# Performance work log

Hardware: AMD Instinct MI355X
Metric: run time of the kernel (lower is better)

## Reference

```python
import jax, jax.numpy as jnp
import numpy as np

D = 1024   # n_embd
H = 16     # n_head
NL = 6     # n_layer
B = 16
L = 64
T = 3 * L  # interleaved (rtg, state, action) tokens
NB = 100   # rtg bucket number
DF = 4 * D


def _ln(x, g, b, eps=1e-5):
    mu = jnp.mean(x, -1, keepdims=True)
    var = jnp.mean((x - mu) ** 2, -1, keepdims=True)
    return (x - mu) * jax.lax.rsqrt(var + eps) * g + b


def _gelu(x):
    return jax.nn.gelu(x, approximate=False)  # matches torch F.gelu (erf)


def setup_inputs() -> dict:
    key = jax.random.key(0)
    ks = iter(jax.random.split(key, 64))
    def rn(shape, s=0.02):
        return jax.random.normal(next(ks), shape, jnp.float32) * s
    inp = dict(
        states=jax.random.normal(next(ks), (B, L, 91), jnp.float32),
        actions=jax.random.normal(next(ks), (B, L, 1, 27), jnp.float32),
        rtgs=jax.random.uniform(next(ks), (B, L), jnp.float32) * 100.0,
        attention_mask=jnp.ones((B, L), bool),
        y_len=L,
        # state encoder: Linear(91,D) GELU Linear(D,D) GELU
        se_w1=rn((91, D)), se_b1=jnp.zeros(D), se_w2=rn((D, D)), se_b2=jnp.zeros(D),
        # action encoder: Linear(27,D) GELU Linear(D,D)
        ae_w1=rn((27, D)), ae_b1=jnp.zeros(D), ae_w2=rn((D, D)), ae_b2=jnp.zeros(D),
        # Autodis
        ad_bucket_w=rn((1, D)), ad_bucket_b=jnp.zeros(D), ad_ret_w=rn((1, NB)), ad_res_w=rn((NB, NB)),
        pos_emb=rn((1, T, D)),
        # transformer blocks (stacked over layers)
        ln1_g=jnp.ones((NL, D)), ln1_b=jnp.zeros((NL, D)),
        Wq=rn((NL, D, D)), bq=jnp.zeros((NL, D)),
        Wk=rn((NL, D, D)), bk=jnp.zeros((NL, D)),
        Wv=rn((NL, D, D)), bv=jnp.zeros((NL, D)),
        Wp=rn((NL, D, D)), bp=jnp.zeros((NL, D)),
        ln2_g=jnp.ones((NL, D)), ln2_b=jnp.zeros((NL, D)),
        Wm1=rn((NL, D, DF)), bm1=jnp.zeros((NL, DF)),
        Wm2=rn((NL, DF, D)), bm2=jnp.zeros((NL, D)),
        lin_w=rn((D, 27)), lin_b=jnp.zeros(27),
    )
    return inp


def _forward(attention_mask, states, actions, rtgs, se_w1, se_b1, se_w2, se_b2,
             ae_w1, ae_b1, ae_w2, ae_b2, ad_bucket_w, ad_bucket_b, ad_ret_w, ad_res_w,
             pos_emb, ln1_g, ln1_b, Wq, bq, Wk, bk, Wv, bv, Wp, bp,
             ln2_g, ln2_b, Wm1, bm1, Wm2, bm2, lin_w, lin_b):
    Bsz, Ls = states.shape[0], states.shape[1]
    Ts = 3 * Ls
    hd = D // H
    # encoders
    state_emb = _gelu(_gelu(states @ se_w1 + se_b1) @ se_w2 + se_b2)          # [B,L,D]
    act = actions[:, :, 0, :]                                                  # squeeze(2) -> [B,L,27]
    action_emb = _gelu(act @ ae_w1 + ae_b1) @ ae_w2 + ae_b2                    # [B,L,D]
    # Autodis rtg embedding
    bucket_value = jnp.linspace(0.0, 100.0, NB).reshape(NB, 1)
    meta = bucket_value @ ad_bucket_w + ad_bucket_b                            # [NB,D]
    s = jax.nn.leaky_relu(rtgs[..., None] @ ad_ret_w)                          # [B,L,NB]
    s = s + s @ ad_res_w
    e = jnp.exp(s - jnp.max(s, -1, keepdims=True))
    p = e / (1e-8 + jnp.sum(e, -1, keepdims=True))
    rtg_emb = p @ meta                                                         # [B,L,D]
    # interleave rtg/state/action tokens -> [B,3L,D]
    tok = jnp.stack([rtg_emb, state_emb, action_emb], axis=2).reshape(Bsz, Ts, D)
    x = tok + pos_emb[:, :Ts]
    # combined padding + causal mask
    m = jnp.repeat(attention_mask, 3, axis=1)                                  # [B,3L]
    causal = jnp.tril(jnp.ones((Ts, Ts), bool))
    fmask = m[:, None, :, None] & m[:, None, None, :] & causal[None, None]     # [B,1,T,T]
    scale = 1.0 / np.sqrt(hd)
    for i in range(NL):
        h = _ln(x, ln1_g[i], ln1_b[i])
        q = (h @ Wq[i] + bq[i]).reshape(Bsz, Ts, H, hd).transpose(0, 2, 1, 3)
        k = (h @ Wk[i] + bk[i]).reshape(Bsz, Ts, H, hd).transpose(0, 2, 1, 3)
        v = (h @ Wv[i] + bv[i]).reshape(Bsz, Ts, H, hd).transpose(0, 2, 1, 3)
        att = jnp.einsum('bhid,bhjd->bhij', q, k) * scale
        att = jnp.where(fmask, att, -1e9)
        att = jax.nn.softmax(att, axis=-1)
        y = jnp.einsum('bhij,bhjd->bhid', att, v).transpose(0, 2, 1, 3).reshape(Bsz, Ts, D)
        x = x + (y @ Wp[i] + bp[i])
        h2 = _ln(x, ln2_g[i], ln2_b[i])
        x = x + _gelu(h2 @ Wm1[i] + bm1[i]) @ Wm2[i] + bm2[i]
    return x @ lin_w + lin_b                                                   # [B,3L,27]


def reference(states, actions, rtgs, attention_mask, y_len, se_w1, se_b1, se_w2, se_b2,
              ae_w1, ae_b1, ae_w2, ae_b2, ad_bucket_w, ad_bucket_b, ad_ret_w, ad_res_w,
              pos_emb, ln1_g, ln1_b, Wq, bq, Wk, bk, Wv, bv, Wp, bp,
              ln2_g, ln2_b, Wm1, bm1, Wm2, bm2, lin_w, lin_b):
    return _forward(attention_mask, states, actions, rtgs, se_w1, se_b1, se_w2, se_b2,
                    ae_w1, ae_b1, ae_w2, ae_b2, ad_bucket_w, ad_bucket_b, ad_ret_w, ad_res_w,
                    pos_emb, ln1_g, ln1_b, Wq, bq, Wk, bk, Wv, bv, Wp, bp,
                    ln2_g, ln2_b, Wm1, bm1, Wm2, bm2, lin_w, lin_b)
```

## Files before the change

kernel.cpp:

```cpp
#include <hip/hip_runtime.h>
#include <cmath>

typedef unsigned short u16;
typedef unsigned int   u32;
typedef short s16x8 __attribute__((ext_vector_type(8)));
typedef float f32x4 __attribute__((ext_vector_type(4)));

#define D_  1024
#define H_  16
#define NL_ 6
#define B_  16
#define L_  64
#define T_  192
#define NB_ 100
#define DF_ 4096
#define BT_ (B_*T_)
#define BL_ (B_*L_)

__device__ __forceinline__ float b2f(u16 u){ u32 x = ((u32)u)<<16; return __uint_as_float(x); }
__device__ __forceinline__ u16 f2b(float f){ u32 x = __float_as_uint(f); x += 0x7fffu + ((x>>16)&1u); return (u16)(x>>16); }
__device__ __forceinline__ float gelu_f(float v){ return 0.5f*v*(1.0f+erff(v*0.70710678118f)); }

typedef const unsigned int __attribute__((address_space(1)))* as1_u32p;
typedef unsigned int __attribute__((address_space(3)))* as3_u32p;
__device__ __forceinline__ void gload16(const void* g, void* l)
{
    __builtin_amdgcn_global_load_lds((as1_u32p)g, (as3_u32p)l, 16, 0, 0);
}

__global__ __launch_bounds__(256) void tconv_kernel(const float* __restrict__ W,
                                                    u16* __restrict__ Wt,
                                                    int K, int N,
                                                    size_t inLS, size_t outLS)
{
    __shared__ float tile[64][65];
    int tid = threadIdx.x;
    int nb = blockIdx.x * 64, kb = blockIdx.y * 64;
    const float* Wz = W + blockIdx.z * inLS;
    u16* Wtz = Wt + blockIdx.z * outLS;
    int tr = tid >> 4, tc = tid & 15;
#pragma unroll
    for (int rr = 0; rr < 4; ++rr) {
        int k = tr + rr*16;
        float4 v = *(const float4*)(Wz + (size_t)(kb + k)*N + nb + tc*4);
        tile[k][tc*4+0] = v.x; tile[k][tc*4+1] = v.y;
        tile[k][tc*4+2] = v.z; tile[k][tc*4+3] = v.w;
    }
    __syncthreads();
#pragma unroll
    for (int rr = 0; rr < 4; ++rr) {
        int n = tr + rr*16;
        ushort4 o;
        o.x = f2b(tile[tc*4+0][n]);
        o.y = f2b(tile[tc*4+1][n]);
        o.z = f2b(tile[tc*4+2][n]);
        o.w = f2b(tile[tc*4+3][n]);
        *(ushort4*)(Wtz + (size_t)(nb + n)*K + kb + tc*4) = o;
    }
}

__global__ __launch_bounds__(256) void tconv4_kernel(const float* __restrict__ Wq,
                                                     const float* __restrict__ Wk,
                                                     const float* __restrict__ Wv,
                                                     const float* __restrict__ Wp,
                                                     u16* __restrict__ Wqkvt,
                                                     u16* __restrict__ Wpt)
{
    __shared__ float tile[64][65];
    int tid = threadIdx.x;
    int z = blockIdx.z;
    int sel = z / NL_, layer = z - sel*NL_;
    size_t DD = (size_t)D_*D_;
    const float* Wz = ((sel == 0) ? Wq : (sel == 1) ? Wk : (sel == 2) ? Wv : Wp) + layer*DD;
    u16* Wtz = (sel == 3) ? (Wpt + layer*DD) : (Wqkvt + layer*3*DD + sel*DD);
    int nb = blockIdx.x * 64, kb = blockIdx.y * 64;
    int tr = tid >> 4, tc = tid & 15;
#pragma unroll
    for (int rr = 0; rr < 4; ++rr) {
        int k = tr + rr*16;
        float4 v = *(const float4*)(Wz + (size_t)(kb + k)*D_ + nb + tc*4);
        tile[k][tc*4+0] = v.x; tile[k][tc*4+1] = v.y;
        tile[k][tc*4+2] = v.z; tile[k][tc*4+3] = v.w;
    }
    __syncthreads();
#pragma unroll
    for (int rr = 0; rr < 4; ++rr) {
        int n = tr + rr*16;
        ushort4 o;
        o.x = f2b(tile[tc*4+0][n]);
        o.y = f2b(tile[tc*4+1][n]);
        o.z = f2b(tile[tc*4+2][n]);
        o.w = f2b(tile[tc*4+3][n]);
        *(ushort4*)(Wtz + (size_t)(nb + n)*D_ + kb + tc*4) = o;
    }
}

__global__ __launch_bounds__(256) void pack_qkv_bias_kernel(const float* __restrict__ bq,
                                                            const float* __restrict__ bk,
                                                            const float* __restrict__ bv,
                                                            float* __restrict__ out)
{
    int i = blockIdx.x*256 + threadIdx.x;
    int layer = i / 3072;
    int r = i - layer*3072;
    int c = r >> 10, d = r & 1023;
    const float* src = (c == 0) ? bq : (c == 1) ? bk : bv;
    out[i] = src[layer*1024 + d];
}

__global__ __launch_bounds__(256) void tlin_kernel(const float* __restrict__ w,
                                                   float* __restrict__ wt)
{
    int k = blockIdx.x*256 + threadIdx.x;
#pragma unroll 1
    for (int c = 0; c < 27; ++c)
        wt[c*1024 + k] = w[k*27 + c];
}

__global__ __launch_bounds__(256) void embed1_kernel(const float* __restrict__ A,
                                                     const float* __restrict__ W,
                                                     const float* __restrict__ bias,
                                                     u16* __restrict__ out, int K)
{
    int idx = blockIdx.x*256 + threadIdx.x;
    int m = idx >> 10, n = idx & 1023;
    float acc = bias[n];
    for (int k = 0; k < K; ++k)
        acc += A[m*K + k] * W[k*1024 + n];
    out[idx] = f2b(gelu_f(acc));
}

__global__ __launch_bounds__(128) void rtg_kernel(const float* __restrict__ rtgs,
                                                  const float* __restrict__ ret_w,
                                                  const float* __restrict__ res_w,
                                                  const float* __restrict__ bucket_w,
                                                  const float* __restrict__ bucket_b,
                                                  float* __restrict__ eR)
{
    int r = blockIdx.x, tid = threadIdx.x;
    __shared__ float sarr[NB_];
    __shared__ float red[128];
    float rtg = rtgs[r];
    float s = 0.f;
    if (tid < NB_) {
        float v = rtg * ret_w[tid];
        s = (v > 0.f) ? v : 0.01f*v;
        sarr[tid] = s;
    }
    __syncthreads();
    float s2 = -1e30f;
    if (tid < NB_) {
        float acc = s;
        for (int m = 0; m < NB_; ++m) acc += sarr[m] * res_w[m*NB_ + tid];
        s2 = acc;
    }
    red[tid] = s2; __syncthreads();
    for (int off = 64; off > 0; off >>= 1) { if (tid < off) red[tid] = fmaxf(red[tid], red[tid+off]); __syncthreads(); }
    float mx = red[0]; __syncthreads();
    float e = (tid < NB_) ? expf(s2 - mx) : 0.f;
    red[tid] = e; __syncthreads();
    for (int off = 64; off > 0; off >>= 1) { if (tid < off) red[tid] += red[tid+off]; __syncthreads(); }
    float S = red[0]; __syncthreads();
    float bv = (100.f/99.f) * (float)tid;
    red[tid] = e * bv; __syncthreads();
    for (int off = 64; off > 0; off >>= 1) { if (tid < off) red[tid] += red[tid+off]; __syncthreads(); }
    float EB = red[0];
    float inv = 1.f/(1e-8f + S);
    float c = EB * inv, sg = S * inv;
    for (int d = tid; d < D_; d += 128)
        eR[(size_t)r*D_ + d] = c*bucket_w[d] + sg*bucket_b[d];
}

__global__ __launch_bounds__(256) void assemble_kernel(const float* __restrict__ eR,
                                                       const float* __restrict__ eS,
                                                       const float* __restrict__ eA,
                                                       const float* __restrict__ pos,
                                                       float* __restrict__ xf)
{
    int idx = blockIdx.x*256 + threadIdx.x;
    int row = idx >> 10, d = idx & 1023;
    int b = row / T_, t = row % T_;
    int l = t / 3, c = t % 3;
    const float* src = (c == 0) ? eR : (c == 1) ? eS : eA;
    xf[idx] = src[(size_t)(b*L_ + l)*D_ + d] + pos[(size_t)t*D_ + d];
}

template<int NP>
__global__ __launch_bounds__(256) void ln_kernel(const float* __restrict__ x,
                                                 const float* __restrict__ p0,
                                                 const float* __restrict__ p1,
                                                 const float* __restrict__ g,
                                                 const float* __restrict__ bb,
                                                 float* __restrict__ xout,
                                                 u16* __restrict__ out)
{
    int row = blockIdx.x, tid = threadIdx.x;
    int lane = tid & 63, wv = tid >> 6;
    __shared__ float ps[8];
    float4 v = ((const float4*)(x + (size_t)row*D_))[tid];
    if (NP == 2) {
        float4 a = ((const float4*)(p0 + (size_t)row*D_))[tid];
        float4 b = ((const float4*)(p1 + (size_t)row*D_))[tid];
        v.x += a.x + b.x; v.y += a.y + b.y; v.z += a.z + b.z; v.w += a.w + b.w;
        ((float4*)(xout + (size_t)row*D_))[tid] = v;
    }
    float s = v.x+v.y+v.z+v.w;
    float q = v.x*v.x+v.y*v.y+v.z*v.z+v.w*v.w;
#pragma unroll
    for (int off = 1; off < 64; off <<= 1) {
        s += __shfl_xor(s, off, 64);
        q += __shfl_xor(q, off, 64);
    }
    if (lane == 0) { ps[wv] = s; ps[4+wv] = q; }
    __syncthreads();
    s = ps[0]+ps[1]+ps[2]+ps[3];
    q = ps[4]+ps[5]+ps[6]+ps[7];
    float mean = s*(1.f/(float)D_);
    float var  = q*(1.f/(float)D_) - mean*mean;
    float rstd = rsqrtf(var + 1e-5f);
    int d0 = tid*4;
    ushort4 ov;
    ov.x = f2b((v.x-mean)*rstd*g[d0+0] + bb[d0+0]);
    ov.y = f2b((v.y-mean)*rstd*g[d0+1] + bb[d0+1]);
    ov.z = f2b((v.z-mean)*rstd*g[d0+2] + bb[d0+2]);
    ov.w = f2b((v.w-mean)*rstd*g[d0+3] + bb[d0+3]);
    ((ushort4*)(out + (size_t)row*D_))[tid] = ov;
}

template<int GELU_ACT, int SPLITK, int ATOMIC>
__global__ __launch_bounds__(256) void gemm_bt(const u16* __restrict__ A,
                                               const u16* __restrict__ Bt,
                                               const float* __restrict__ bias,
                                               float* __restrict__ outF,
                                               u16* __restrict__ outB,
                                               int M, int N, int K, int kc,
                                               size_t partStride)
{
    __shared__ __align__(16) u16 As[3*128*32];
    __shared__ __align__(16) u16 Bs[3*128*32];
    int tid = threadIdx.x;

    int gx = gridDim.x;
    int nwg = gx * gridDim.y;
    int id = blockIdx.y * gx + blockIdx.x;
    int q8 = nwg >> 3;
    int nid = (id & 7) * q8 + (id >> 3);
    int n0 = (nid % gx) * 128;
    int m0 = (nid / gx) * 128;

    int wave = tid >> 6, lane = tid & 63;
    int wm = (wave >> 1) * 64, wn = (wave & 1) * 64;
    int lr = lane & 15, lq = lane >> 4;
    int slotRd = (lq ^ ((lr >> 1) & 3)) * 8;

    int srow = tid >> 2;
    int sslot = (tid & 3) ^ ((srow >> 1) & 3);

    int k0 = (SPLITK > 1) ? blockIdx.z * kc : 0;
    int nIt = ((SPLITK > 1) ? kc : K) >> 5;

    const u16* ap0 = A  + (size_t)(m0 + srow) * K + k0 + sslot * 8;
    const u16* ap1 = ap0 + (size_t)64 * K;
    const u16* bp0 = Bt + (size_t)(n0 + srow) * K + k0 + sslot * 8;
    const u16* bp1 = bp0 + (size_t)64 * K;

    u16 *sA0 = As, *sA1 = As + 4096, *sA2 = As + 8192;
    u16 *sB0 = Bs, *sB1 = Bs + 4096, *sB2 = Bs + 8192;
    int woff = wave * 512;

    f32x4 acc[4][4];
#pragma unroll
    for (int i = 0; i < 4; ++i)
#pragma unroll
        for (int j = 0; j < 4; ++j) acc[i][j] = (f32x4){0.f,0.f,0.f,0.f};

    gload16(ap0, sA0 + woff); gload16(ap1, sA0 + 2048 + woff);
    gload16(bp0, sB0 + woff); gload16(bp1, sB0 + 2048 + woff);
    ap0 += 32; ap1 += 32; bp0 += 32; bp1 += 32;
    gload16(ap0, sA1 + woff); gload16(ap1, sA1 + 2048 + woff);
    gload16(bp0, sB1 + woff); gload16(bp1, sB1 + 2048 + woff);
    ap0 += 32; ap1 += 32; bp0 += 32; bp1 += 32;

    for (int it = 0; it < nIt; ++it) {
        if (it + 1 < nIt) asm volatile("s_waitcnt vmcnt(4)" ::: "memory");
        else              asm volatile("s_waitcnt vmcnt(0)" ::: "memory");
        asm volatile("s_barrier" ::: "memory");
        if (it + 2 < nIt) {
            gload16(ap0, sA2 + woff); gload16(ap1, sA2 + 2048 + woff);
            gload16(bp0, sB2 + woff); gload16(bp1, sB2 + 2048 + woff);
            ap0 += 32; ap1 += 32; bp0 += 32; bp1 += 32;
        }
        s16x8 af[4], bf[4];
#pragma unroll
        for (int i = 0; i < 4; ++i)
            af[i] = *(const s16x8*)(sA0 + (wm + i*16 + lr)*32 + slotRd);
#pragma unroll
        for (int j = 0; j < 4; ++j)
            bf[j] = *(const s16x8*)(sB0 + (wn + j*16 + lr)*32 + slotRd);
#pragma unroll
        for (int i = 0; i < 4; ++i)
#pragma unroll
            for (int j = 0; j < 4; ++j)
                acc[i][j] = __builtin_amdgcn_mfma_f32_16x16x32_bf16(af[i], bf[j], acc[i][j], 0, 0, 0);
        u16* t0 = sA0; sA0 = sA1; sA1 = sA2; sA2 = t0;
        u16* t1 = sB0; sB0 = sB1; sB1 = sB2; sB2 = t1;
    }

    float* outZ = (SPLITK > 1 && !ATOMIC) ? outF + (size_t)blockIdx.z * partStride : outF;
#pragma unroll
    for (int i = 0; i < 4; ++i) {
        int mbase = m0 + wm + i*16 + lq*4;
#pragma unroll
        for (int j = 0; j < 4; ++j) {
            int n = n0 + wn + j*16 + lr;
            float bvl = (SPLITK > 1) ? ((blockIdx.z == 0) ? bias[n] : 0.f) : bias[n];
#pragma unroll
            for (int r = 0; r < 4; ++r) {
                int m = mbase + r;
                float v = acc[i][j][r] + bvl;
                size_t off = (size_t)m*N + n;
                if (SPLITK > 1) {
                    if (ATOMIC) atomicAdd(outF + off, v);
                    else        outZ[off] = v;
                } else {
                    if (GELU_ACT) v = gelu_f(v);
                    if (outF) outF[off] = v;
                    if (outB) outB[off] = f2b(v);
                }
            }
        }
    }
}

__global__ __launch_bounds__(256) void attn_mfma_kernel(const u16* __restrict__ qkv,
                                                        u16* __restrict__ yb)
{
    __shared__ __align__(16) u16 Ks[192*72];
    __shared__ __align__(16) u16 Vt[64*200];
    __shared__ __align__(16) u16 Pch[4][16*40];

    int tid = threadIdx.x;
    int b = blockIdx.x >> 4, h = blockIdx.x & 15;
    int c = blockIdx.y;
    int nrows = (c + 1) * 64;
    int bT = b * T_;
    int colBase = h * 64;
    int w = tid >> 6, lane = tid & 63;
    int lr = lane & 15, lq = lane >> 4;
    const int S3 = 3 * D_;

    for (int it = 0; it < (nrows >> 5); ++it) {
        int cc = it*256 + tid;
        int row = cc >> 3, ch = cc & 7;
        *(int4*)(Ks + row*72 + ch*8) =
            *(const int4*)(qkv + (size_t)(bT+row)*S3 + D_ + colBase + ch*8);
        union { int4 v; u16 s[8]; } rv;
        rv.v = *(const int4*)(qkv + (size_t)(bT+row)*S3 + 2*D_ + colBase + ch*8);
#pragma unroll
        for (int i2 = 0; i2 < 8; ++i2)
            Vt[(ch*8 + i2)*200 + row] = rv.s[i2];
    }
    __syncthreads();

    u16* Ch = Pch[w];
    int qt = c*4 + w;
    int tqb = qt * 16;

    const u16* qrow = qkv + (size_t)(bT + tqb + lr)*S3 + colBase + lq*8;
    s16x8 af0 = *(const s16x8*)(qrow);
    s16x8 af1 = *(const s16x8*)(qrow + 32);

    f32x4 sacc[12];
#pragma unroll
    for (int jt = 0; jt < 12; ++jt) {
        if (jt <= qt) {
            s16x8 bk0 = *(const s16x8*)(Ks + (jt*16 + lr)*72 + lq*8);
            s16x8 bk1 = *(const s16x8*)(Ks + (jt*16 + lr)*72 + 32 + lq*8);
            f32x4 a = (f32x4){0.f,0.f,0.f,0.f};
            a = __builtin_amdgcn_mfma_f32_16x16x32_bf16(af0, bk0, a, 0, 0, 0);
            a = __builtin_amdgcn_mfma_f32_16x16x32_bf16(af1, bk1, a, 0, 0, 0);
            sacc[jt] = a;
        }
    }

    float mrow[4] = {-1e30f,-1e30f,-1e30f,-1e30f};
#pragma unroll
    for (int jt = 0; jt < 12; ++jt) if (jt <= qt) {
#pragma unroll
        for (int r = 0; r < 4; ++r) {
            bool valid = (jt < qt) || (lr <= lq*4 + r);
            float s = valid ? sacc[jt][r]*0.125f : -1e30f;
            sacc[jt][r] = s;
            mrow[r] = fmaxf(mrow[r], s);
        }
    }
#pragma unroll
    for (int r = 0; r < 4; ++r) {
#pragma unroll
        for (int off = 1; off < 16; off <<= 1)
            mrow[r] = fmaxf(mrow[r], __shfl_xor(mrow[r], off, 64));
    }

    float lrow[4] = {0.f,0.f,0.f,0.f};
#pragma unroll
    for (int jt = 0; jt < 12; ++jt) if (jt <= qt) {
#pragma unroll
        for (int r = 0; r < 4; ++r) {
            float e = __expf(sacc[jt][r] - mrow[r]);
            sacc[jt][r] = e;
            lrow[r] += e;
        }
    }
#pragma unroll
    for (int r = 0; r < 4; ++r) {
#pragma unroll
        for (int off = 1; off < 16; off <<= 1)
            lrow[r] += __shfl_xor(lrow[r], off, 64);
        lrow[r] = 1.f / lrow[r];
    }

    int nkt = (qt + 2) >> 1;
    f32x4 oacc[4];
#pragma unroll
    for (int nt = 0; nt < 4; ++nt) oacc[nt] = (f32x4){0.f,0.f,0.f,0.f};

#pragma unroll
    for (int kt = 0; kt < 6; ++kt) if (kt < nkt) {
        int jt0 = 2*kt, jt1 = 2*kt + 1;
#pragma unroll
        for (int r = 0; r < 4; ++r) {
            u16 e0 = f2b(sacc[jt0][r]);
            u16 e1 = (jt1 <= qt) ? f2b(sacc[jt1][r]) : (u16)0;
            Ch[(lq*4 + r)*40 + lr]      = e0;
            Ch[(lq*4 + r)*40 + 16 + lr] = e1;
        }
        s16x8 ap = *(const s16x8*)(Ch + lr*40 + lq*8);
#pragma unroll
        for (int nt = 0; nt < 4; ++nt) {
            s16x8 bv = *(const s16x8*)(Vt + (nt*16 + lr)*200 + kt*32 + lq*8);
            oacc[nt] = __builtin_amdgcn_mfma_f32_16x16x32_bf16(ap, bv, oacc[nt], 0, 0, 0);
        }
    }

#pragma unroll
    for (int nt = 0; nt < 4; ++nt)
#pragma unroll
        for (int r = 0; r < 4; ++r)
            yb[(size_t)(bT + tqb + lq*4 + r)*D_ + colBase + nt*16 + lr] =
                f2b(oacc[nt][r] * lrow[r]);
}

template<int NP>
__global__ __launch_bounds__(256) void final_kernel(const float* __restrict__ xf,
                                                    const float* __restrict__ q0,
                                                    const float* __restrict__ q1,
                                                    const float* __restrict__ lin_wT,
                                                    const float* __restrict__ lin_b,
                                                    float* __restrict__ out)
{
    int row = blockIdx.x*4 + (threadIdx.x >> 6);
    int lane = threadIdx.x & 63;
    const float4* xr = (const float4*)(xf + (size_t)row*D_);
    float4 x[4];
#pragma unroll
    for (int i = 0; i < 4; ++i) {
        float4 v = xr[lane + i*64];
        if (NP == 2) {
            float4 a = ((const float4*)(q0 + (size_t)row*D_))[lane + i*64];
            float4 b = ((const float4*)(q1 + (size_t)row*D_))[lane + i*64];
            v.x += a.x + b.x; v.y += a.y + b.y; v.z += a.z + b.z; v.w += a.w + b.w;
        }
        x[i] = v;
    }
#pragma unroll 1
    for (int c = 0; c < 27; ++c) {
        const float4* wr = (const float4*)(lin_wT + (size_t)c*D_);
        float a = 0.f;
#pragma unroll
        for (int i = 0; i < 4; ++i) {
            float4 wv = wr[lane + i*64];
            a += x[i].x*wv.x + x[i].y*wv.y + x[i].z*wv.z + x[i].w*wv.w;
        }
#pragma unroll
        for (int off = 1; off < 64; off <<= 1)
            a += __shfl_xor(a, off, 64);
        if (lane == 0) out[(size_t)row*27 + c] = a + lin_b[c];
    }
}

extern "C" void kernel_launch(void* const* d_in, const int* in_sizes, int n_in,
                              void* d_out, int out_size, void* d_ws, size_t ws_size,
                              hipStream_t stream)
{
    const float* states   = (const float*)d_in[0];
    const float* actions  = (const float*)d_in[1];
    const float* rtgs     = (const float*)d_in[2];
    const float* se_w1 = (const float*)d_in[5];
    const float* se_b1 = (const float*)d_in[6];
    const float* se_w2 = (const float*)d_in[7];
    const float* se_b2 = (const float*)d_in[8];
    const float* ae_w1 = (const float*)d_in[9];
    const float* ae_b1 = (const float*)d_in[10];
    const float* ae_w2 = (const float*)d_in[11];
    const float* ae_b2 = (const float*)d_in[12];
    const float* ad_bucket_w = (const float*)d_in[13];
    const float* ad_bucket_b = (const float*)d_in[14];
    const float* ad_ret_w = (const float*)d_in[15];
    const float* ad_res_w = (const float*)d_in[16];
    const float* pos_emb  = (const float*)d_in[17];
    const float* ln1_g = (const float*)d_in[18];
    const float* ln1_b = (const float*)d_in[19];
    const float* Wq = (const float*)d_in[20];
    const float* bq = (const float*)d_in[21];
    const float* Wk = (const float*)d_in[22];
    const float* bk = (const float*)d_in[23];
    const float* Wv = (const float*)d_in[24];
    const float* bv = (const float*)d_in[25];
    const float* Wp = (const float*)d_in[26];
    const float* bp = (const float*)d_in[27];
    const float* ln2_g = (const float*)d_in[28];
    const float* ln2_b = (const float*)d_in[29];
    const float* Wm1 = (const float*)d_in[30];
    const float* bm1 = (const float*)d_in[31];
    const float* Wm2 = (const float*)d_in[32];
    const float* bm2 = (const float*)d_in[33];
    const float* lin_w = (const float*)d_in[34];
    const float* lin_b = (const float*)d_in[35];

    char* w = (char*)d_ws;
    auto take = [&](size_t bytes) { char* p = w; w += (bytes + 255) & ~(size_t)255; return p; };

    float* xf   = (float*)take((size_t)BT_*D_*4);
    u16* hb     = (u16*)take((size_t)BT_*D_*2);
    char* qkvr  =        take((size_t)2*BT_*D_*4);
    u16*  qkvb  = (u16*)qkvr;
    float* mq0  = (float*)qkvr;
    float* mq1  = (float*)(qkvr + (size_t)BT_*D_*4);
    char* scr   =        take((size_t)BT_*DF_*2);
    u16*  midb  = (u16*)scr;
    float* pp0  = (float*)scr;
    float* pp1  = (float*)(scr + (size_t)BT_*D_*4);
    u16*  tSb   = (u16*)scr;
    u16*  tAb   = (u16*)(scr + (size_t)BL_*D_*2);
    float* eS   = (float*)(scr + (size_t)2*BL_*D_*2);
    float* eA   = (float*)(scr + (size_t)2*BL_*D_*2 + (size_t)BL_*D_*4);
    float* eR   = (float*)(scr + (size_t)2*BL_*D_*2 + (size_t)2*BL_*D_*4);

    u16* Wqkvt = (u16*)take((size_t)NL_*3*D_*D_*2);
    u16* Wpt   = (u16*)take((size_t)NL_*D_*D_*2);
    u16* Wm1t  = (u16*)take((size_t)NL_*D_*DF_*2);
    u16* Wm2t  = (u16*)take((size_t)NL_*DF_*D_*2);
    u16* sw2t  = (u16*)take((size_t)D_*D_*2);
    u16* aw2t  = (u16*)take((size_t)D_*D_*2);
    float* bqkv= (float*)take((size_t)NL_*3*D_*4);
    float* lwT = (float*)take((size_t)27*D_*4);

    size_t ask = (size_t)(w - (char*)d_ws);
    bool bigWS = (ws_size >= ask);

    const size_t PSTRIDE = (size_t)BT_*D_;

    size_t DD = (size_t)D_*D_, DDF = (size_t)D_*DF_;
    tconv4_kernel<<<dim3(16,16,4*NL_), 256, 0, stream>>>(Wq, Wk, Wv, Wp, Wqkvt, Wpt);
    tconv_kernel<<<dim3(64,16,NL_), 256, 0, stream>>>(Wm1, Wm1t, D_,  DF_, DDF, DDF);
    tconv_kernel<<<dim3(16,64,NL_), 256, 0, stream>>>(Wm2, Wm2t, DF_, D_,  DDF, DDF);
    tconv_kernel<<<dim3(16,16,1),   256, 0, stream>>>(se_w2, sw2t, D_, D_, 0, 0);
    tconv_kernel<<<dim3(16,16,1),   256, 0, stream>>>(ae_w2, aw2t, D_, D_, 0, 0);
    pack_qkv_bias_kernel<<<72, 256, 0, stream>>>(bq, bk, bv, bqkv);
    tlin_kernel<<<4, 256, 0, stream>>>(lin_w, lwT);

    embed1_kernel<<<4096, 256, 0, stream>>>(states,  se_w1, se_b1, tSb, 91);
    embed1_kernel<<<4096, 256, 0, stream>>>(actions, ae_w1, ae_b1, tAb, 27);
    gemm_bt<1,1,0><<<dim3(8,8), 256, 0, stream>>>(tSb, sw2t, se_b2, eS, nullptr, BL_, D_, D_, D_, 0);
    gemm_bt<0,1,0><<<dim3(8,8), 256, 0, stream>>>(tAb, aw2t, ae_b2, eA, nullptr, BL_, D_, D_, D_, 0);
    rtg_kernel<<<BL_, 128, 0, stream>>>(rtgs, ad_ret_w, ad_res_w, ad_bucket_w, ad_bucket_b, eR);
    assemble_kernel<<<(BT_*D_)/256, 256, 0, stream>>>(eR, eS, eA, pos_emb, xf);

    for (int i = 0; i < NL_; ++i) {
        if (i > 0 && bigWS)
            ln_kernel<2><<<BT_, 256, 0, stream>>>(xf, mq0, mq1, ln1_g + i*D_, ln1_b + i*D_, xf, hb);
        else
            ln_kernel<0><<<BT_, 256, 0, stream>>>(xf, nullptr, nullptr, ln1_g + i*D_, ln1_b + i*D_, nullptr, hb);
        gemm_bt<0,1,0><<<dim3(24,24), 256, 0, stream>>>(hb, Wqkvt + (size_t)i*3*DD, bqkv + i*3*D_,
                                                        nullptr, qkvb, BT_, 3*D_, D_, D_, 0);
        attn_mfma_kernel<<<dim3(B_*H_,3), 256, 0, stream>>>(qkvb, hb);
        gemm_bt<0,2,0><<<dim3(8,24,2), 256, 0, stream>>>(hb, Wpt + (size_t)i*DD, bp + i*D_,
                                                         pp0, nullptr, BT_, D_, D_, 512, PSTRIDE);
        ln_kernel<2><<<BT_, 256, 0, stream>>>(xf, pp0, pp1, ln2_g + i*D_, ln2_b + i*D_, xf, hb);
        gemm_bt<1,1,0><<<dim3(32,24), 256, 0, stream>>>(hb, Wm1t + (size_t)i*DDF, bm1 + i*DF_,
                                                        nullptr, midb, BT_, DF_, D_, D_, 0);
        if (bigWS)
            gemm_bt<0,2,0><<<dim3(8,24,2), 256, 0, stream>>>(midb, Wm2t + (size_t)i*DDF, bm2 + i*D_,
                                                             mq0, nullptr, BT_, D_, DF_, 2048, PSTRIDE);
        else
            gemm_bt<0,2,1><<<dim3(8,24,2), 256, 0, stream>>>(midb, Wm2t + (size_t)i*DDF, bm2 + i*D_,
                                                             xf, nullptr, BT_, D_, DF_, 2048, 0);
    }

    if (bigWS)
        final_kernel<2><<<BT_/4, 256, 0, stream>>>(xf, mq0, mq1, lwT, lin_b, (float*)d_out);
    else
        final_kernel<0><<<BT_/4, 256, 0, stream>>>(xf, nullptr, nullptr, lwT, lin_b, (float*)d_out);
}
```

Measured before the change: 1.597 ms.

## Split-K by 4 for projection GEMMs, per-layer weight conversion, wave-per-row layernorm

```diff
diff --git a/kernel.cpp b/kernel.cpp
--- a/kernel.cpp
+++ b/kernel.cpp
@@ -28,21 +28,16 @@
     __builtin_amdgcn_global_load_lds((as1_u32p)g, (as3_u32p)l, 16, 0, 0);
 }
 
-__global__ __launch_bounds__(256) void tconv_kernel(const float* __restrict__ W,
-                                                    u16* __restrict__ Wt,
-                                                    int K, int N,
-                                                    size_t inLS, size_t outLS)
+__device__ __forceinline__ void tconv_tile(const float* __restrict__ W,
+                                           u16* __restrict__ Wt,
+                                           int K, int N, int nb, int kb, int tid)
 {
     __shared__ float tile[64][65];
-    int tid = threadIdx.x;
-    int nb = blockIdx.x * 64, kb = blockIdx.y * 64;
-    const float* Wz = W + blockIdx.z * inLS;
-    u16* Wtz = Wt + blockIdx.z * outLS;
     int tr = tid >> 4, tc = tid & 15;
 #pragma unroll
     for (int rr = 0; rr < 4; ++rr) {
         int k = tr + rr*16;
-        float4 v = *(const float4*)(Wz + (size_t)(kb + k)*N + nb + tc*4);
+        float4 v = *(const float4*)(W + (size_t)(kb + k)*N + nb + tc*4);
         tile[k][tc*4+0] = v.x; tile[k][tc*4+1] = v.y;
         tile[k][tc*4+2] = v.z; tile[k][tc*4+3] = v.w;
     }
@@ -55,43 +50,47 @@
         o.y = f2b(tile[tc*4+1][n]);
         o.z = f2b(tile[tc*4+2][n]);
         o.w = f2b(tile[tc*4+3][n]);
-        *(ushort4*)(Wtz + (size_t)(nb + n)*K + kb + tc*4) = o;
-    }
-}
-
-__global__ __launch_bounds__(256) void tconv4_kernel(const float* __restrict__ Wq,
-                                                     const float* __restrict__ Wk,
-                                                     const float* __restrict__ Wv,
-                                                     const float* __restrict__ Wp,
-                                                     u16* __restrict__ Wqkvt,
-                                                     u16* __restrict__ Wpt)
-{
-    __shared__ float tile[64][65];
-    int tid = threadIdx.x;
-    int z = blockIdx.z;
-    int sel = z / NL_, layer = z - sel*NL_;
+        *(ushort4*)(Wt + (size_t)(nb + n)*K + kb + tc*4) = o;
+    }
+}
+
+__global__ __launch_bounds__(256) void tconv_kernel(const float* __restrict__ W,
+                                                    u16* __restrict__ Wt,
+                                                    int K, int N)
+{
+    tconv_tile(W, Wt, K, N, blockIdx.x*64, blockIdx.y*64, threadIdx.x);
+}
+
+__global__ __launch_bounds__(256) void tconv4L_kernel(const float* __restrict__ Wq,
+                                                      const float* __restrict__ Wk,
+                                                      const float* __restrict__ Wv,
+                                                      const float* __restrict__ Wp,
+                                                      u16* __restrict__ Wqkvt,
+                                                      u16* __restrict__ Wpt,
+                                                      int layer)
+{
+    int sel = blockIdx.z;
     size_t DD = (size_t)D_*D_;
     const float* Wz = ((sel == 0) ? Wq : (sel == 1) ? Wk : (sel == 2) ? Wv : Wp) + layer*DD;
     u16* Wtz = (sel == 3) ? (Wpt + layer*DD) : (Wqkvt + layer*3*DD + sel*DD);
-    int nb = blockIdx.x * 64, kb = blockIdx.y * 64;
-    int tr = tid >> 4, tc = tid & 15;
-#pragma unroll
-    for (int rr = 0; rr < 4; ++rr) {
-        int k = tr + rr*16;
-        float4 v = *(const float4*)(Wz + (size_t)(kb + k)*D_ + nb + tc*4);
-        tile[k][tc*4+0] = v.x; tile[k][tc*4+1] = v.y;
-        tile[k][tc*4+2] = v.z; tile[k][tc*4+3] = v.w;
-    }
-    __syncthreads();
-#pragma unroll
-    for (int rr = 0; rr < 4; ++rr) {
-        int n = tr + rr*16;
-        ushort4 o;
-        o.x = f2b(tile[tc*4+0][n]);
-        o.y = f2b(tile[tc*4+1][n]);
-        o.z = f2b(tile[tc*4+2][n]);
-        o.w = f2b(tile[tc*4+3][n]);
-        *(ushort4*)(Wtz + (size_t)(nb + n)*D_ + kb + tc*4) = o;
+    tconv_tile(Wz, Wtz, D_, D_, blockIdx.x*64, blockIdx.y*64, threadIdx.x);
+}
+
+__global__ __launch_bounds__(256) void tconv_mlpL_kernel(const float* __restrict__ Wm1,
+                                                         const float* __restrict__ Wm2,
+                                                         u16* __restrict__ Wm1t,
+                                                         u16* __restrict__ Wm2t,
+                                                         int layer)
+{
+    size_t DDF = (size_t)D_*DF_;
+    int t = blockIdx.x;
+    if (t < 1024) {
+        int nbi = t & 63, kbi = t >> 6;
+        tconv_tile(Wm1 + layer*DDF, Wm1t + layer*DDF, D_, DF_, nbi*64, kbi*64, threadIdx.x);
+    } else {
+        int t2 = t - 1024;
+        int nbi = t2 & 15, kbi = t2 >> 4;
+        tconv_tile(Wm2 + layer*DDF, Wm2t + layer*DDF, DF_, D_, nbi*64, kbi*64, threadIdx.x);
     }
 }
 
@@ -187,44 +186,55 @@
 
 template<int NP>
 __global__ __launch_bounds__(256) void ln_kernel(const float* __restrict__ x,
-                                                 const float* __restrict__ p0,
-                                                 const float* __restrict__ p1,
+                                                 const float* __restrict__ parts,
+                                                 size_t pstride,
                                                  const float* __restrict__ g,
                                                  const float* __restrict__ bb,
                                                  float* __restrict__ xout,
                                                  u16* __restrict__ out)
 {
-    int row = blockIdx.x, tid = threadIdx.x;
-    int lane = tid & 63, wv = tid >> 6;
-    __shared__ float ps[8];
-    float4 v = ((const float4*)(x + (size_t)row*D_))[tid];
-    if (NP == 2) {
-        float4 a = ((const float4*)(p0 + (size_t)row*D_))[tid];
-        float4 b = ((const float4*)(p1 + (size_t)row*D_))[tid];
-        v.x += a.x + b.x; v.y += a.y + b.y; v.z += a.z + b.z; v.w += a.w + b.w;
-        ((float4*)(xout + (size_t)row*D_))[tid] = v;
-    }
-    float s = v.x+v.y+v.z+v.w;
-    float q = v.x*v.x+v.y*v.y+v.z*v.z+v.w*v.w;
+    int row = blockIdx.x*4 + (threadIdx.x >> 6);
+    int lane = threadIdx.x & 63;
+    const float4* xr = (const float4*)(x + (size_t)row*D_);
+    float4 v[4];
+    float s = 0.f, q = 0.f;
+#pragma unroll
+    for (int i = 0; i < 4; ++i) {
+        float4 a = xr[lane + i*64];
+        if (NP == 4) {
+#pragma unroll
+            for (int z = 0; z < 4; ++z) {
+                float4 p = ((const float4*)(parts + (size_t)z*pstride + (size_t)row*D_))[lane + i*64];
+                a.x += p.x; a.y += p.y; a.z += p.z; a.w += p.w;
+            }
+        }
+        v[i] = a;
+        s += a.x+a.y+a.z+a.w;
+        q += a.x*a.x+a.y*a.y+a.z*a.z+a.w*a.w;
+    }
+    if (NP == 4) {
+#pragma unroll
+        for (int i = 0; i < 4; ++i)
+            ((float4*)(xout + (size_t)row*D_))[lane + i*64] = v[i];
+    }
 #pragma unroll
     for (int off = 1; off < 64; off <<= 1) {
         s += __shfl_xor(s, off, 64);
         q += __shfl_xor(q, off, 64);
     }
-    if (lane == 0) { ps[wv] = s; ps[4+wv] = q; }
-    __syncthreads();
-    s = ps[0]+ps[1]+ps[2]+ps[3];
-    q = ps[4]+ps[5]+ps[6]+ps[7];
     float mean = s*(1.f/(float)D_);
     float var  = q*(1.f/(float)D_) - mean*mean;
     float rstd = rsqrtf(var + 1e-5f);
-    int d0 = tid*4;
-    ushort4 ov;
-    ov.x = f2b((v.x-mean)*rstd*g[d0+0] + bb[d0+0]);
-    ov.y = f2b((v.y-mean)*rstd*g[d0+1] + bb[d0+1]);
-    ov.z = f2b((v.z-mean)*rstd*g[d0+2] + bb[d0+2]);
-    ov.w = f2b((v.w-mean)*rstd*g[d0+3] + bb[d0+3]);
-    ((ushort4*)(out + (size_t)row*D_))[tid] = ov;
+#pragma unroll
+    for (int i = 0; i < 4; ++i) {
+        int d0 = (lane + i*64)*4;
+        ushort4 ov;
+        ov.x = f2b((v[i].x-mean)*rstd*g[d0+0] + bb[d0+0]);
+        ov.y = f2b((v[i].y-mean)*rstd*g[d0+1] + bb[d0+1]);
+        ov.z = f2b((v[i].z-mean)*rstd*g[d0+2] + bb[d0+2]);
+        ov.w = f2b((v[i].w-mean)*rstd*g[d0+3] + bb[d0+3]);
+        ((ushort4*)(out + (size_t)row*D_))[lane + i*64] = ov;
+    }
 }
 
 template<int GELU_ACT, int SPLITK, int ATOMIC>
@@ -452,8 +462,8 @@
 
 template<int NP>
 __global__ __launch_bounds__(256) void final_kernel(const float* __restrict__ xf,
-                                                    const float* __restrict__ q0,
-                                                    const float* __restrict__ q1,
+                                                    const float* __restrict__ parts,
+                                                    size_t pstride,
                                                     const float* __restrict__ lin_wT,
                                                     const float* __restrict__ lin_b,
                                                     float* __restrict__ out)
@@ -465,10 +475,12 @@
 #pragma unroll
     for (int i = 0; i < 4; ++i) {
         float4 v = xr[lane + i*64];
-        if (NP == 2) {
-            float4 a = ((const float4*)(q0 + (size_t)row*D_))[lane + i*64];
-            float4 b = ((const float4*)(q1 + (size_t)row*D_))[lane + i*64];
-            v.x += a.x + b.x; v.y += a.y + b.y; v.z += a.z + b.z; v.w += a.w + b.w;
+        if (NP == 4) {
+#pragma unroll
+            for (int z = 0; z < 4; ++z) {
+                float4 p = ((const float4*)(parts + (size_t)z*pstride + (size_t)row*D_))[lane + i*64];
+                v.x += p.x; v.y += p.y; v.z += p.z; v.w += p.w;
+            }
         }
         x[i] = v;
     }
@@ -532,19 +544,16 @@
 
     float* xf   = (float*)take((size_t)BT_*D_*4);
     u16* hb     = (u16*)take((size_t)BT_*D_*2);
-    char* qkvr  =        take((size_t)2*BT_*D_*4);
-    u16*  qkvb  = (u16*)qkvr;
-    float* mq0  = (float*)qkvr;
-    float* mq1  = (float*)(qkvr + (size_t)BT_*D_*4);
+    u16* qkvb   = (u16*)take((size_t)BT_*3*D_*2);
     char* scr   =        take((size_t)BT_*DF_*2);
     u16*  midb  = (u16*)scr;
-    float* pp0  = (float*)scr;
-    float* pp1  = (float*)(scr + (size_t)BT_*D_*4);
     u16*  tSb   = (u16*)scr;
     u16*  tAb   = (u16*)(scr + (size_t)BL_*D_*2);
     float* eS   = (float*)(scr + (size_t)2*BL_*D_*2);
     float* eA   = (float*)(scr + (size_t)2*BL_*D_*2 + (size_t)BL_*D_*4);
     float* eR   = (float*)(scr + (size_t)2*BL_*D_*2 + (size_t)2*BL_*D_*4);
+    float* pp   = (float*)take((size_t)4*BT_*D_*4);
+    float* mq   = (float*)take((size_t)4*BT_*D_*4);
 
     u16* Wqkvt = (u16*)take((size_t)NL_*3*D_*D_*2);
     u16* Wpt   = (u16*)take((size_t)NL_*D_*D_*2);
@@ -559,15 +568,14 @@
     bool bigWS = (ws_size >= ask);
 
     const size_t PSTRIDE = (size_t)BT_*D_;
-
     size_t DD = (size_t)D_*D_, DDF = (size_t)D_*DF_;
-    tconv4_kernel<<<dim3(16,16,4*NL_), 256, 0, stream>>>(Wq, Wk, Wv, Wp, Wqkvt, Wpt);
-    tconv_kernel<<<dim3(64,16,NL_), 256, 0, stream>>>(Wm1, Wm1t, D_,  DF_, DDF, DDF);
-    tconv_kernel<<<dim3(16,64,NL_), 256, 0, stream>>>(Wm2, Wm2t, DF_, D_,  DDF, DDF);
-    tconv_kernel<<<dim3(16,16,1),   256, 0, stream>>>(se_w2, sw2t, D_, D_, 0, 0);
-    tconv_kernel<<<dim3(16,16,1),   256, 0, stream>>>(ae_w2, aw2t, D_, D_, 0, 0);
+
     pack_qkv_bias_kernel<<<72, 256, 0, stream>>>(bq, bk, bv, bqkv);
     tlin_kernel<<<4, 256, 0, stream>>>(lin_w, lwT);
+    tconv_kernel<<<dim3(16,16), 256, 0, stream>>>(se_w2, sw2t, D_, D_);
+    tconv_kernel<<<dim3(16,16), 256, 0, stream>>>(ae_w2, aw2t, D_, D_);
+    tconv4L_kernel<<<dim3(16,16,4), 256, 0, stream>>>(Wq, Wk, Wv, Wp, Wqkvt, Wpt, 0);
+    tconv_mlpL_kernel<<<2048, 256, 0, stream>>>(Wm1, Wm2, Wm1t, Wm2t, 0);
 
     embed1_kernel<<<4096, 256, 0, stream>>>(states,  se_w1, se_b1, tSb, 91);
     embed1_kernel<<<4096, 256, 0, stream>>>(actions, ae_w1, ae_b1, tAb, 27);
@@ -578,27 +586,38 @@
 
     for (int i = 0; i < NL_; ++i) {
         if (i > 0 && bigWS)
-            ln_kernel<2><<<BT_, 256, 0, stream>>>(xf, mq0, mq1, ln1_g + i*D_, ln1_b + i*D_, xf, hb);
+            ln_kernel<4><<<BT_/4, 256, 0, stream>>>(xf, mq, PSTRIDE, ln1_g + i*D_, ln1_b + i*D_, xf, hb);
         else
-            ln_kernel<0><<<BT_, 256, 0, stream>>>(xf, nullptr, nullptr, ln1_g + i*D_, ln1_b + i*D_, nullptr, hb);
+            ln_kernel<0><<<BT_/4, 256, 0, stream>>>(xf, nullptr, 0, ln1_g + i*D_, ln1_b + i*D_, nullptr, hb);
         gemm_bt<0,1,0><<<dim3(24,24), 256, 0, stream>>>(hb, Wqkvt + (size_t)i*3*DD, bqkv + i*3*D_,
                                                         nullptr, qkvb, BT_, 3*D_, D_, D_, 0);
         attn_mfma_kernel<<<dim3(B_*H_,3), 256, 0, stream>>>(qkvb, hb);
-        gemm_bt<0,2,0><<<dim3(8,24,2), 256, 0, stream>>>(hb, Wpt + (size_t)i*DD, bp + i*D_,
-                                                         pp0, nullptr, BT_, D_, D_, 512, PSTRIDE);
-        ln_kernel<2><<<BT_, 256, 0, stream>>>(xf, pp0, pp1, ln2_g + i*D_, ln2_b + i*D_, xf, hb);
+        if (i + 1 < NL_)
+            tconv4L_kernel<<<dim3(16,16,4), 256, 0, stream>>>(Wq, Wk, Wv, Wp, Wqkvt, Wpt, i+1);
+        if (bigWS)
+            gemm_bt<0,4,0><<<dim3(8,24,4), 256, 0, stream>>>(hb, Wpt + (size_t)i*DD, bp + i*D_,
+                                                             pp, nullptr, BT_, D_, D_, 256, PSTRIDE);
+        else
+            gemm_bt<0,2,1><<<dim3(8,24,2), 256, 0, stream>>>(hb, Wpt + (size_t)i*DD, bp + i*D_,
+                                                             xf, nullptr, BT_, D_, D_, 512, 0);
+        if (bigWS)
+            ln_kernel<4><<<BT_/4, 256, 0, stream>>>(xf, pp, PSTRIDE, ln2_g + i*D_, ln2_b + i*D_, xf, hb);
+        else
+            ln_kernel<0><<<BT_/4, 256, 0, stream>>>(xf, nullptr, 0, ln2_g + i*D_, ln2_b + i*D_, nullptr, hb);
         gemm_bt<1,1,0><<<dim3(32,24), 256, 0, stream>>>(hb, Wm1t + (size_t)i*DDF, bm1 + i*DF_,
                                                         nullptr, midb, BT_, DF_, D_, D_, 0);
         if (bigWS)
-            gemm_bt<0,2,0><<<dim3(8,24,2), 256, 0, stream>>>(midb, Wm2t + (size_t)i*DDF, bm2 + i*D_,
-                                                             mq0, nullptr, BT_, D_, DF_, 2048, PSTRIDE);
+            gemm_bt<0,4,0><<<dim3(8,24,4), 256, 0, stream>>>(midb, Wm2t + (size_t)i*DDF, bm2 + i*D_,
+                                                             mq, nullptr, BT_, D_, DF_, 1024, PSTRIDE);
         else
             gemm_bt<0,2,1><<<dim3(8,24,2), 256, 0, stream>>>(midb, Wm2t + (size_t)i*DDF, bm2 + i*D_,
                                                              xf, nullptr, BT_, D_, DF_, 2048, 0);
+        if (i + 1 < NL_)
+            tconv_mlpL_kernel<<<2048, 256, 0, stream>>>(Wm1, Wm2, Wm1t, Wm2t, i+1);
     }
 
     if (bigWS)
-        final_kernel<2><<<BT_/4, 256, 0, stream>>>(xf, mq0, mq1, lwT, lin_b, (float*)d_out);
+        final_kernel<4><<<BT_/4, 256, 0, stream>>>(xf, mq, PSTRIDE, lwT, lin_b, (float*)d_out);
     else
-        final_kernel<0><<<BT_/4, 256, 0, stream>>>(xf, nullptr, nullptr, lwT, lin_b, (float*)d_out);
-}
+        final_kernel<0><<<BT_/4, 256, 0, stream>>>(xf, nullptr, 0, lwT, lin_b, (float*)d_out);
+}
```

After: 1.534 ms. 3.9% less time.
